# Kernel optimization log

Measured on AMD Instinct MI355X. Metric: run time of the kernel, lower is better.

## Reference

```python
import jax, jax.numpy as jnp
import numpy as np

N = 100_000      # nodes
E = 1_600_000    # edges (avg degree 16)
EP = 500_000     # pos/neg decode edges each
IN, H, OUT = 256, 128, 64


def setup_inputs() -> dict:
    key = jax.random.key(0)
    ks = jax.random.split(key, 8)
    x = jax.random.normal(ks[0], (N, IN), dtype=jnp.float32)
    edge_index = jax.random.randint(ks[1], (2, E), 0, N, dtype=jnp.int32)
    pos_edge_index = jax.random.randint(ks[2], (2, EP), 0, N, dtype=jnp.int32)
    neg_edge_index = jax.random.randint(ks[3], (2, EP), 0, N, dtype=jnp.int32)
    W1 = jax.random.normal(ks[4], (IN, H), dtype=jnp.float32) * (1.0 / np.sqrt(IN))
    b1 = jnp.zeros((H,), dtype=jnp.float32)
    W2 = jax.random.normal(ks[5], (H, OUT), dtype=jnp.float32) * (1.0 / np.sqrt(H))
    b2 = jnp.zeros((OUT,), dtype=jnp.float32)
    return dict(x=x, edge_index=edge_index, pos_edge_index=pos_edge_index,
                neg_edge_index=neg_edge_index, W1=W1, b1=b1, W2=W2, b2=b2)


def _gcn_conv(x, src, dst, norm, W, b, n_nodes):
    # PyG GCNConv: linear transform, then normalized scatter-add aggregation
    h = x @ W                              # [N, out]
    msg = h[src] * norm[:, None]           # gather + scale, [E+N, out]
    agg = jax.ops.segment_sum(msg, dst, num_segments=n_nodes)
    return agg + b


def reference(x, edge_index, pos_edge_index, neg_edge_index, W1, b1, W2, b2):
    n = x.shape[0]
    loops = jnp.arange(n, dtype=edge_index.dtype)
    src = jnp.concatenate([edge_index[0], loops])   # add self-loops (GCNConv default)
    dst = jnp.concatenate([edge_index[1], loops])
    # symmetric normalization D^{-1/2} (A+I) D^{-1/2}
    deg = jax.ops.segment_sum(jnp.ones_like(src, dtype=x.dtype), dst, num_segments=n)
    dinv = jnp.where(deg > 0, jax.lax.rsqrt(jnp.maximum(deg, 1e-12)), 0.0)
    norm = dinv[src] * dinv[dst]
    # encode
    h = jax.nn.relu(_gcn_conv(x, src, dst, norm, W1, b1, n))
    z = _gcn_conv(h, src, dst, norm, W2, b2, n)
    # decode: edge score = <z_u, z_v> over pos+neg edges
    ei = jnp.concatenate([pos_edge_index, neg_edge_index], axis=-1)
    return (z[ei[0]] * z[ei[1]]).sum(axis=-1)   # [2*EP]
```

## Files before the change

kernel.cpp:

```cpp
#include <hip/hip_runtime.h>


#define BUK_SHIFT 7
#define BUK_NODES 128

__global__ __launch_bounds__(256) void b_hist_k(const int* __restrict__ dst, int E,
                                                int nbuk, int* __restrict__ bhist) {
  __shared__ int h[1024];
  for (int i = threadIdx.x; i < nbuk; i += 256) h[i] = 0;
  __syncthreads();
  for (int i = blockIdx.x * 256 + threadIdx.x; i < E; i += gridDim.x * 256)
    atomicAdd(&h[dst[i] >> BUK_SHIFT], 1);
  __syncthreads();
  for (int i = threadIdx.x; i < nbuk; i += 256) {
    int c = h[i];
    if (c) atomicAdd(&bhist[i], c);
  }
}

__global__ __launch_bounds__(256) void b_scan_k(const int* __restrict__ bhist,
                                                int nbuk, int* __restrict__ bbase,
                                                int* __restrict__ bcur) {
  __shared__ int arr[256];
  const int t = threadIdx.x;
  const int per = (nbuk + 255) / 256;
  const int start = t * per;
  const int end = min(start + per, nbuk);
  int s = 0;
  for (int i = start; i < end; ++i) s += bhist[i];
  arr[t] = s;
  __syncthreads();
  for (int off = 1; off < 256; off <<= 1) {
    int v = (t >= off) ? arr[t - off] : 0;
    __syncthreads();
    arr[t] += v;
    __syncthreads();
  }
  int run = arr[t] - s;
  for (int i = start; i < end; ++i) {
    bbase[i] = run;
    bcur[i] = run;
    run += bhist[i];
  }
  if (t == 255) bbase[nbuk] = arr[255];
}

__global__ __launch_bounds__(256) void b_scatter_k(const int* __restrict__ src,
                                                   const int* __restrict__ dst, int E,
                                                   int nbuk, int* __restrict__ bcur,
                                                   int* __restrict__ ebuf) {
  __shared__ int lh[1024];
  __shared__ int lc[1024];
  const int base = blockIdx.x * 8192;
  if (base >= E) return;
  const int end = min(base + 8192, E);
  for (int i = threadIdx.x; i < nbuk; i += 256) lh[i] = 0;
  __syncthreads();
  for (int i = base + threadIdx.x; i < end; i += 256)
    atomicAdd(&lh[dst[i] >> BUK_SHIFT], 1);
  __syncthreads();
  for (int i = threadIdx.x; i < nbuk; i += 256) {
    int c = lh[i];
    lc[i] = c ? atomicAdd(&bcur[i], c) : 0;
  }
  __syncthreads();
  for (int i = base + threadIdx.x; i < end; i += 256) {
    int d = dst[i];
    int pos = atomicAdd(&lc[d >> BUK_SHIFT], 1);
    ebuf[pos] = src[i] | ((d & (BUK_NODES - 1)) << 17);
  }
}

__global__ __launch_bounds__(128) void b_build_k(const int* __restrict__ ebuf,
                                                 const int* __restrict__ bbase, int n,
                                                 int nbuk, float* __restrict__ dinv,
                                                 int* __restrict__ rowptr,
                                                 int* __restrict__ csr) {
  __shared__ int cnt[BUK_NODES];
  __shared__ int pre[BUK_NODES];
  __shared__ int cur[BUK_NODES];
  const int b = blockIdx.x, t = threadIdx.x;
  cnt[t] = 0;
  __syncthreads();
  const int beg = bbase[b], end = bbase[b + 1];
  for (int i = beg + t; i < end; i += 128) atomicAdd(&cnt[ebuf[i] >> 17], 1);
  __syncthreads();
  const int c = cnt[t];
  pre[t] = c;
  __syncthreads();
  for (int off = 1; off < 128; off <<= 1) {
    int v = (t >= off) ? pre[t - off] : 0;
    __syncthreads();
    pre[t] += v;
    __syncthreads();
  }
  const int base = beg + pre[t] - c;
  cur[t] = base;
  const int node = (b << BUK_SHIFT) + t;
  if (node < n) {
    rowptr[node] = base;
    dinv[node] = rsqrtf((float)(c + 1));
  }
  if (b == 0 && t == 0) rowptr[n] = bbase[nbuk];
  __syncthreads();
  for (int i = beg + t; i < end; i += 128) {
    int e = ebuf[i];
    int pos = atomicAdd(&cur[e >> 17], 1);
    csr[pos] = e & 0x1FFFF;
  }
}

template <int BM, int BN, int BK, int TM, int TN>
__global__ __launch_bounds__(256) void gemm_tiled(const float* __restrict__ A,
                                                  const float* __restrict__ B,
                                                  float* __restrict__ C,
                                                  const float* __restrict__ rowscale,
                                                  int M, int K) {
  __shared__ float As[BK][BM + 4];
  __shared__ float Bs[BK * BN];
  const int tid = threadIdx.x;
  const int tx = tid % (BN / TN);
  const int ty = tid / (BN / TN);
  const int lane = tid & 63;
  const int wave = tid >> 6;
  const int rowBase = blockIdx.x * BM;

  float acc[TM][TN];
#pragma unroll
  for (int i = 0; i < TM; ++i)
#pragma unroll
    for (int j = 0; j < TN; ++j) acc[i][j] = 0.f;

  constexpr int BS_BYTES = BK * BN * 4;
  constexpr int CALLS = BS_BYTES / 4096;

  for (int k0 = 0; k0 < K; k0 += BK) {
    {
      const char* gsrc = (const char*)(B + (size_t)k0 * BN);
#pragma unroll
      for (int q = 0; q < CALLS; ++q) {
        const int off = wave * (CALLS * 1024) + q * 1024 + lane * 16;
        __builtin_amdgcn_global_load_lds(
            (const __attribute__((address_space(1))) void*)(gsrc + off),
            (__attribute__((address_space(3))) void*)((char*)Bs + off), 16, 0, 0);
      }
    }
#pragma unroll
    for (int l = 0; l < BM * BK / (4 * 256); ++l) {
      const int idx = tid + l * 256;
      const int arow = idx / (BK / 4);
      const int acol = (idx % (BK / 4)) * 4;
      const int gr = rowBase + arow;
      float4 v;
      if (gr < M)
        v = *reinterpret_cast<const float4*>(&A[(size_t)gr * K + k0 + acol]);
      else
        v = make_float4(0.f, 0.f, 0.f, 0.f);
      As[acol + 0][arow] = v.x;
      As[acol + 1][arow] = v.y;
      As[acol + 2][arow] = v.z;
      As[acol + 3][arow] = v.w;
    }
    __syncthreads();
#pragma unroll
    for (int kk = 0; kk < BK; ++kk) {
      float ra[TM], rb[TN];
#pragma unroll
      for (int i = 0; i < TM; i += 4)
        *reinterpret_cast<float4*>(&ra[i]) =
            *reinterpret_cast<const float4*>(&As[kk][ty * TM + i]);
#pragma unroll
      for (int j = 0; j < TN; j += 4)
        *reinterpret_cast<float4*>(&rb[j]) =
            *reinterpret_cast<const float4*>(&Bs[kk * BN + tx * TN + j]);
#pragma unroll
      for (int i = 0; i < TM; ++i)
#pragma unroll
        for (int j = 0; j < TN; ++j) acc[i][j] += ra[i] * rb[j];
    }
    __syncthreads();
  }
#pragma unroll
  for (int i = 0; i < TM; ++i) {
    const int gr = rowBase + ty * TM + i;
    if (gr < M) {
      const float s = rowscale[gr];
#pragma unroll
      for (int j = 0; j < TN; j += 4) {
        float4 v = {acc[i][j] * s, acc[i][j + 1] * s, acc[i][j + 2] * s,
                    acc[i][j + 3] * s};
        *reinterpret_cast<float4*>(&C[(size_t)gr * BN + tx * TN + j]) = v;
      }
    }
  }
}

template <bool RELU>
__global__ __launch_bounds__(256) void agg128_k(const float* __restrict__ g,
                                                const int* __restrict__ rowptr,
                                                const int* __restrict__ csr,
                                                const float* __restrict__ dinv,
                                                const float* __restrict__ bias,
                                                float* __restrict__ hout, int n) {
  const int wid = (blockIdx.x * 256 + threadIdx.x) >> 6;
  if (wid >= n) return;
  const int lane = threadIdx.x & 63;
  const int half = lane >> 5;
  const size_t col = (size_t)(lane & 31) * 4;
  const float dd = dinv[wid];
  const int beg = rowptr[wid];
  const int end = rowptr[wid + 1];
  float4 acc = make_float4(0.f, 0.f, 0.f, 0.f);
  int e = beg;
  for (; e + 8 <= end; e += 8) {
    const int s0 = csr[e + 0 + half];
    const int s1 = csr[e + 2 + half];
    const int s2 = csr[e + 4 + half];
    const int s3 = csr[e + 6 + half];
    const float4 v0 = *reinterpret_cast<const float4*>(&g[(size_t)s0 * 128 + col]);
    const float4 v1 = *reinterpret_cast<const float4*>(&g[(size_t)s1 * 128 + col]);
    const float4 v2 = *reinterpret_cast<const float4*>(&g[(size_t)s2 * 128 + col]);
    const float4 v3 = *reinterpret_cast<const float4*>(&g[(size_t)s3 * 128 + col]);
    acc.x += (v0.x + v1.x) + (v2.x + v3.x);
    acc.y += (v0.y + v1.y) + (v2.y + v3.y);
    acc.z += (v0.z + v1.z) + (v2.z + v3.z);
    acc.w += (v0.w + v1.w) + (v2.w + v3.w);
  }
  for (; e + 2 <= end; e += 2) {
    const int s = csr[e + half];
    const float4 v = *reinterpret_cast<const float4*>(&g[(size_t)s * 128 + col]);
    acc.x += v.x;
    acc.y += v.y;
    acc.z += v.z;
    acc.w += v.w;
  }
  if (e < end && half == 0) {
    const int s = csr[e];
    const float4 v = *reinterpret_cast<const float4*>(&g[(size_t)s * 128 + col]);
    acc.x += v.x;
    acc.y += v.y;
    acc.z += v.z;
    acc.w += v.w;
  }
  acc.x += __shfl_xor(acc.x, 32);
  acc.y += __shfl_xor(acc.y, 32);
  acc.z += __shfl_xor(acc.z, 32);
  acc.w += __shfl_xor(acc.w, 32);
  if (half == 0) {
    const float4 sv = *reinterpret_cast<const float4*>(&g[(size_t)wid * 128 + col]);
    const float4 b = *reinterpret_cast<const float4*>(&bias[col]);
    float4 r;
    r.x = dd * (acc.x + sv.x) + b.x;
    r.y = dd * (acc.y + sv.y) + b.y;
    r.z = dd * (acc.z + sv.z) + b.z;
    r.w = dd * (acc.w + sv.w) + b.w;
    if (RELU) {
      r.x = fmaxf(r.x, 0.f);
      r.y = fmaxf(r.y, 0.f);
      r.z = fmaxf(r.z, 0.f);
      r.w = fmaxf(r.w, 0.f);
    }
    *reinterpret_cast<float4*>(&hout[(size_t)wid * 128 + col]) = r;
  }
}

__global__ __launch_bounds__(256) void agg64_k(const float* __restrict__ g,
                                               const int* __restrict__ rowptr,
                                               const int* __restrict__ csr,
                                               const float* __restrict__ dinv,
                                               const float* __restrict__ bias,
                                               float* __restrict__ hout, int n) {
  const int wid = (blockIdx.x * 256 + threadIdx.x) >> 6;
  if (wid >= n) return;
  const int lane = threadIdx.x & 63;
  const int quad = lane >> 4;
  const size_t col = (size_t)(lane & 15) * 4;
  const float dd = dinv[wid];
  const int beg = rowptr[wid];
  const int end = rowptr[wid + 1];
  float4 acc = make_float4(0.f, 0.f, 0.f, 0.f);
  int e = beg;
  for (; e + 16 <= end; e += 16) {
    const int s0 = csr[e + 0 + quad];
    const int s1 = csr[e + 4 + quad];
    const int s2 = csr[e + 8 + quad];
    const int s3 = csr[e + 12 + quad];
    const float4 v0 = *reinterpret_cast<const float4*>(&g[(size_t)s0 * 64 + col]);
    const float4 v1 = *reinterpret_cast<const float4*>(&g[(size_t)s1 * 64 + col]);
    const float4 v2 = *reinterpret_cast<const float4*>(&g[(size_t)s2 * 64 + col]);
    const float4 v3 = *reinterpret_cast<const float4*>(&g[(size_t)s3 * 64 + col]);
    acc.x += (v0.x + v1.x) + (v2.x + v3.x);
    acc.y += (v0.y + v1.y) + (v2.y + v3.y);
    acc.z += (v0.z + v1.z) + (v2.z + v3.z);
    acc.w += (v0.w + v1.w) + (v2.w + v3.w);
  }
  for (; e + 4 <= end; e += 4) {
    const int s = csr[e + quad];
    const float4 v = *reinterpret_cast<const float4*>(&g[(size_t)s * 64 + col]);
    acc.x += v.x;
    acc.y += v.y;
    acc.z += v.z;
    acc.w += v.w;
  }
  const int r = end - e;
  if (quad < r) {
    const int s = csr[e + quad];
    const float4 v = *reinterpret_cast<const float4*>(&g[(size_t)s * 64 + col]);
    acc.x += v.x;
    acc.y += v.y;
    acc.z += v.z;
    acc.w += v.w;
  }
  acc.x += __shfl_xor(acc.x, 16);
  acc.y += __shfl_xor(acc.y, 16);
  acc.z += __shfl_xor(acc.z, 16);
  acc.w += __shfl_xor(acc.w, 16);
  acc.x += __shfl_xor(acc.x, 32);
  acc.y += __shfl_xor(acc.y, 32);
  acc.z += __shfl_xor(acc.z, 32);
  acc.w += __shfl_xor(acc.w, 32);
  if (quad == 0) {
    const float4 sv = *reinterpret_cast<const float4*>(&g[(size_t)wid * 64 + col]);
    const float4 b = *reinterpret_cast<const float4*>(&bias[col]);
    float4 res;
    res.x = dd * (acc.x + sv.x) + b.x;
    res.y = dd * (acc.y + sv.y) + b.y;
    res.z = dd * (acc.z + sv.z) + b.z;
    res.w = dd * (acc.w + sv.w) + b.w;
    *reinterpret_cast<float4*>(&hout[(size_t)wid * 64 + col]) = res;
  }
}

__global__ __launch_bounds__(256) void decode_k(const int* __restrict__ pos,
                                                const int* __restrict__ neg,
                                                const float* __restrict__ z,
                                                float* __restrict__ out, int EP) {
  const long long t = (long long)blockIdx.x * 256 + threadIdx.x;
  const long long e = t >> 3;
  const int lane = (int)(t & 7);
  if (e >= 2LL * EP) return;
  int u, v;
  if (e < EP) {
    u = pos[e];
    v = pos[EP + e];
  } else {
    u = neg[e - EP];
    v = neg[EP + (e - EP)];
  }
  const float* zu = &z[(size_t)u * 64 + lane * 8];
  const float* zv = &z[(size_t)v * 64 + lane * 8];
  const float4 a0 = *reinterpret_cast<const float4*>(zu);
  const float4 a1 = *reinterpret_cast<const float4*>(zu + 4);
  const float4 b0 = *reinterpret_cast<const float4*>(zv);
  const float4 b1 = *reinterpret_cast<const float4*>(zv + 4);
  float p = a0.x * b0.x + a0.y * b0.y + a0.z * b0.z + a0.w * b0.w +
            a1.x * b1.x + a1.y * b1.y + a1.z * b1.z + a1.w * b1.w;
#pragma unroll
  for (int off = 4; off > 0; off >>= 1) p += __shfl_down(p, off, 8);
  if (lane == 0) out[e] = p;
}


extern "C" void kernel_launch(void* const* d_in, const int* in_sizes, int n_in,
                              void* d_out, int out_size, void* d_ws, size_t ws_size,
                              hipStream_t stream) {
  const float* x = (const float*)d_in[0];
  const int* ei = (const int*)d_in[1];
  const int* pos = (const int*)d_in[2];
  const int* neg = (const int*)d_in[3];
  const float* W1 = (const float*)d_in[4];
  const float* b1 = (const float*)d_in[5];
  const float* W2 = (const float*)d_in[6];
  const float* b2 = (const float*)d_in[7];
  float* out = (float*)d_out;

  const int H = in_sizes[5];
  const int IN = in_sizes[4] / H;
  const int OUT = in_sizes[7];
  const int N = in_sizes[0] / IN;
  const int E = in_sizes[1] / 2;
  const int EP = in_sizes[2] / 2;
  (void)OUT;

  char* ws = (char*)d_ws;
  size_t off = 0;
  auto carve = [&](size_t bytes) -> char* {
    char* p = ws + off;
    off += (bytes + 255) & ~(size_t)255;
    return p;
  };
  const int NBUK = (N + BUK_NODES - 1) >> BUK_SHIFT;

  float* dinvb = (float*)carve((size_t)N * 4);
  int* rowptr = (int*)carve((size_t)(N + 1) * 4);
  int* bhist = (int*)carve((size_t)NBUK * 4);
  int* bbase = (int*)carve((size_t)(NBUK + 1) * 4);
  int* bcur = (int*)carve((size_t)NBUK * 4);
  int* ebuf = (int*)carve((size_t)E * 4);
  int* csr = (int*)carve((size_t)E * 4);
  float* bufA = (float*)carve((size_t)N * H * 4);
  float* bufB = (float*)carve((size_t)N * H * 4);
  (void)ws_size;

  const int* srcp = ei;
  const int* dstp = ei + E;

  hipMemsetAsync(bhist, 0, (size_t)NBUK * 4, stream);
  b_hist_k<<<512, 256, 0, stream>>>(dstp, E, NBUK, bhist);
  b_scan_k<<<1, 256, 0, stream>>>(bhist, NBUK, bbase, bcur);
  b_scatter_k<<<(E + 8191) / 8192, 256, 0, stream>>>(srcp, dstp, E, NBUK, bcur, ebuf);
  b_build_k<<<NBUK, 128, 0, stream>>>(ebuf, bbase, N, NBUK, dinvb, rowptr, csr);

  gemm_tiled<64, 128, 32, 8, 4>
      <<<(N + 63) / 64, 256, 0, stream>>>(x, W1, bufA, dinvb, N, IN);
  agg128_k<true><<<(N + 3) / 4, 256, 0, stream>>>(bufA, rowptr, csr, dinvb, b1,
                                                  bufB, N);
  gemm_tiled<64, 64, 32, 4, 4>
      <<<(N + 63) / 64, 256, 0, stream>>>(bufB, W2, bufA, dinvb, N, H);
  agg64_k<<<(N + 3) / 4, 256, 0, stream>>>(bufA, rowptr, csr, dinvb, b2, bufB, N);
  const long long threads = 2LL * EP * 8;
  decode_k<<<(int)((threads + 255) / 256), 256, 0, stream>>>(pos, neg, bufB, out, EP);
}
```

Measured before the change: 430.6 us.

## Replace FP32 SIMT GEMMs with split-bf16 MFMA GEMMs

Both dense transforms now run on bf16 MFMA instructions, with an fp32-like result recovered by splitting each operand into hi and lo bf16 parts and issuing three MFMAs (hi*hi, lo*hi, hi*lo). The weights are pre-split and transposed by a small kernel launched on every call. A tiles are converted to hi/lo in registers before being stored to LDS. This targets the FP32 FMA throughput limit of the tiled SIMT GEMM, at the cost of extra conversion work, two extra tiny launches, and slightly different rounding.

```diff
diff --git a/kernel.cpp b/kernel.cpp
--- a/kernel.cpp
+++ b/kernel.cpp
@@ -1,5 +1,8 @@
 #include <hip/hip_runtime.h>
 
+
+typedef __attribute__((ext_vector_type(8))) short short8;
+typedef __attribute__((ext_vector_type(4))) float f32x4;
 
 #define BUK_SHIFT 7
 #define BUK_NODES 128
@@ -110,87 +113,107 @@
   }
 }
 
-template <int BM, int BN, int BK, int TM, int TN>
-__global__ __launch_bounds__(256) void gemm_tiled(const float* __restrict__ A,
-                                                  const float* __restrict__ B,
-                                                  float* __restrict__ C,
-                                                  const float* __restrict__ rowscale,
-                                                  int M, int K) {
-  __shared__ float As[BK][BM + 4];
-  __shared__ float Bs[BK * BN];
+__global__ __launch_bounds__(256) void split_w_k(const float* __restrict__ W, int K,
+                                                 int N,
+                                                 unsigned short* __restrict__ hi,
+                                                 unsigned short* __restrict__ lo) {
+  const int idx = blockIdx.x * 256 + threadIdx.x;
+  if (idx >= K * N) return;
+  const int k = idx / N, c = idx - k * N;
+  const float a = W[idx];
+  const unsigned u = __float_as_uint(a);
+  const unsigned short h = (unsigned short)(u >> 16);
+  const float l = a - __uint_as_float(u & 0xFFFF0000u);
+  const unsigned short lb = (unsigned short)(__float_as_uint(l) >> 16);
+  hi[(size_t)c * K + k] = h;
+  lo[(size_t)c * K + k] = lb;
+}
+
+template <int BN>
+__global__ __launch_bounds__(256) void gemm_mfma(
+    const float* __restrict__ A, const unsigned short* __restrict__ Bthi,
+    const unsigned short* __restrict__ Btlo, float* __restrict__ C,
+    const float* __restrict__ rowscale, int M, int K) {
+  constexpr int BM = 64, BK = 32;
+  constexpr int NT = BN / 16;
+  constexpr int LD = 40;
+  __shared__ unsigned short Ahi[BM * LD];
+  __shared__ unsigned short Alo[BM * LD];
+  __shared__ unsigned short Bhi[BN * LD];
+  __shared__ unsigned short Blo[BN * LD];
   const int tid = threadIdx.x;
-  const int tx = tid % (BN / TN);
-  const int ty = tid / (BN / TN);
   const int lane = tid & 63;
   const int wave = tid >> 6;
   const int rowBase = blockIdx.x * BM;
 
-  float acc[TM][TN];
-#pragma unroll
-  for (int i = 0; i < TM; ++i)
-#pragma unroll
-    for (int j = 0; j < TN; ++j) acc[i][j] = 0.f;
-
-  constexpr int BS_BYTES = BK * BN * 4;
-  constexpr int CALLS = BS_BYTES / 4096;
+  f32x4 acc[NT];
+#pragma unroll
+  for (int c = 0; c < NT; ++c) acc[c] = (f32x4){0.f, 0.f, 0.f, 0.f};
+
+  const int sr = tid >> 2;
+  const int sk = (tid & 3) * 8;
+  const int arow = wave * 16 + (lane & 15);
+  const int akb = (lane >> 4) * 8;
 
   for (int k0 = 0; k0 < K; k0 += BK) {
     {
-      const char* gsrc = (const char*)(B + (size_t)k0 * BN);
-#pragma unroll
-      for (int q = 0; q < CALLS; ++q) {
-        const int off = wave * (CALLS * 1024) + q * 1024 + lane * 16;
-        __builtin_amdgcn_global_load_lds(
-            (const __attribute__((address_space(1))) void*)(gsrc + off),
-            (__attribute__((address_space(3))) void*)((char*)Bs + off), 16, 0, 0);
+      const int gr = rowBase + sr;
+      float4 v0 = make_float4(0.f, 0.f, 0.f, 0.f);
+      float4 v1 = make_float4(0.f, 0.f, 0.f, 0.f);
+      if (gr < M) {
+        const float* p = A + (size_t)gr * K + k0 + sk;
+        v0 = *reinterpret_cast<const float4*>(p);
+        v1 = *reinterpret_cast<const float4*>(p + 4);
       }
+      const float vv[8] = {v0.x, v0.y, v0.z, v0.w, v1.x, v1.y, v1.z, v1.w};
+      short8 hv, lv;
+#pragma unroll
+      for (int i = 0; i < 8; ++i) {
+        const unsigned u = __float_as_uint(vv[i]);
+        hv[i] = (short)(u >> 16);
+        const float l = vv[i] - __uint_as_float(u & 0xFFFF0000u);
+        lv[i] = (short)(__float_as_uint(l) >> 16);
+      }
+      *reinterpret_cast<short8*>(&Ahi[sr * LD + sk]) = hv;
+      *reinterpret_cast<short8*>(&Alo[sr * LD + sk]) = lv;
     }
-#pragma unroll
-    for (int l = 0; l < BM * BK / (4 * 256); ++l) {
-      const int idx = tid + l * 256;
-      const int arow = idx / (BK / 4);
-      const int acol = (idx % (BK / 4)) * 4;
-      const int gr = rowBase + arow;
-      float4 v;
-      if (gr < M)
-        v = *reinterpret_cast<const float4*>(&A[(size_t)gr * K + k0 + acol]);
-      else
-        v = make_float4(0.f, 0.f, 0.f, 0.f);
-      As[acol + 0][arow] = v.x;
-      As[acol + 1][arow] = v.y;
-      As[acol + 2][arow] = v.z;
-      As[acol + 3][arow] = v.w;
+    for (int i = tid; i < BN * 2; i += 256) {
+      const int col = i >> 1;
+      const int kk = (i & 1) * 16;
+      const size_t gofs = (size_t)col * K + k0 + kk;
+      *reinterpret_cast<short8*>(&Bhi[col * LD + kk]) =
+          *reinterpret_cast<const short8*>(&Bthi[gofs]);
+      *reinterpret_cast<short8*>(&Bhi[col * LD + kk + 8]) =
+          *reinterpret_cast<const short8*>(&Bthi[gofs + 8]);
+      *reinterpret_cast<short8*>(&Blo[col * LD + kk]) =
+          *reinterpret_cast<const short8*>(&Btlo[gofs]);
+      *reinterpret_cast<short8*>(&Blo[col * LD + kk + 8]) =
+          *reinterpret_cast<const short8*>(&Btlo[gofs + 8]);
     }
     __syncthreads();
-#pragma unroll
-    for (int kk = 0; kk < BK; ++kk) {
-      float ra[TM], rb[TN];
-#pragma unroll
-      for (int i = 0; i < TM; i += 4)
-        *reinterpret_cast<float4*>(&ra[i]) =
-            *reinterpret_cast<const float4*>(&As[kk][ty * TM + i]);
-#pragma unroll
-      for (int j = 0; j < TN; j += 4)
-        *reinterpret_cast<float4*>(&rb[j]) =
-            *reinterpret_cast<const float4*>(&Bs[kk * BN + tx * TN + j]);
-#pragma unroll
-      for (int i = 0; i < TM; ++i)
-#pragma unroll
-        for (int j = 0; j < TN; ++j) acc[i][j] += ra[i] * rb[j];
+    const short8 fa_hi = *reinterpret_cast<const short8*>(&Ahi[arow * LD + akb]);
+    const short8 fa_lo = *reinterpret_cast<const short8*>(&Alo[arow * LD + akb]);
+#pragma unroll
+    for (int c = 0; c < NT; ++c) {
+      const int bofs = (c * 16 + (lane & 15)) * LD + akb;
+      const short8 fb_hi = *reinterpret_cast<const short8*>(&Bhi[bofs]);
+      const short8 fb_lo = *reinterpret_cast<const short8*>(&Blo[bofs]);
+      acc[c] = __builtin_amdgcn_mfma_f32_16x16x32_bf16(fa_hi, fb_hi, acc[c], 0, 0, 0);
+      acc[c] = __builtin_amdgcn_mfma_f32_16x16x32_bf16(fa_lo, fb_hi, acc[c], 0, 0, 0);
+      acc[c] = __builtin_amdgcn_mfma_f32_16x16x32_bf16(fa_hi, fb_lo, acc[c], 0, 0, 0);
     }
     __syncthreads();
   }
-#pragma unroll
-  for (int i = 0; i < TM; ++i) {
-    const int gr = rowBase + ty * TM + i;
-    if (gr < M) {
-      const float s = rowscale[gr];
-#pragma unroll
-      for (int j = 0; j < TN; j += 4) {
-        float4 v = {acc[i][j] * s, acc[i][j + 1] * s, acc[i][j + 2] * s,
-                    acc[i][j + 3] * s};
-        *reinterpret_cast<float4*>(&C[(size_t)gr * BN + tx * TN + j]) = v;
-      }
+  const int crow = rowBase + wave * 16 + (lane >> 4) * 4;
+  float sc[4];
+#pragma unroll
+  for (int j = 0; j < 4; ++j) sc[j] = (crow + j < M) ? rowscale[crow + j] : 0.f;
+#pragma unroll
+  for (int c = 0; c < NT; ++c) {
+#pragma unroll
+    for (int j = 0; j < 4; ++j) {
+      const int gr = crow + j;
+      if (gr < M) C[(size_t)gr * BN + c * 16 + (lane & 15)] = acc[c][j] * sc[j];
     }
   }
 }
@@ -380,7 +403,6 @@
   const int N = in_sizes[0] / IN;
   const int E = in_sizes[1] / 2;
   const int EP = in_sizes[2] / 2;
-  (void)OUT;
 
   char* ws = (char*)d_ws;
   size_t off = 0;
@@ -400,10 +422,17 @@
   int* csr = (int*)carve((size_t)E * 4);
   float* bufA = (float*)carve((size_t)N * H * 4);
   float* bufB = (float*)carve((size_t)N * H * 4);
+  unsigned short* w1hi = (unsigned short*)carve((size_t)IN * H * 2);
+  unsigned short* w1lo = (unsigned short*)carve((size_t)IN * H * 2);
+  unsigned short* w2hi = (unsigned short*)carve((size_t)H * OUT * 2);
+  unsigned short* w2lo = (unsigned short*)carve((size_t)H * OUT * 2);
   (void)ws_size;
 
   const int* srcp = ei;
   const int* dstp = ei + E;
+
+  split_w_k<<<(IN * H + 255) / 256, 256, 0, stream>>>(W1, IN, H, w1hi, w1lo);
+  split_w_k<<<(H * OUT + 255) / 256, 256, 0, stream>>>(W2, H, OUT, w2hi, w2lo);
 
   hipMemsetAsync(bhist, 0, (size_t)NBUK * 4, stream);
   b_hist_k<<<512, 256, 0, stream>>>(dstp, E, NBUK, bhist);
@@ -411,12 +440,10 @@
   b_scatter_k<<<(E + 8191) / 8192, 256, 0, stream>>>(srcp, dstp, E, NBUK, bcur, ebuf);
   b_build_k<<<NBUK, 128, 0, stream>>>(ebuf, bbase, N, NBUK, dinvb, rowptr, csr);
 
-  gemm_tiled<64, 128, 32, 8, 4>
-      <<<(N + 63) / 64, 256, 0, stream>>>(x, W1, bufA, dinvb, N, IN);
+  gemm_mfma<128><<<(N + 63) / 64, 256, 0, stream>>>(x, w1hi, w1lo, bufA, dinvb, N, IN);
   agg128_k<true><<<(N + 3) / 4, 256, 0, stream>>>(bufA, rowptr, csr, dinvb, b1,
                                                   bufB, N);
-  gemm_tiled<64, 64, 32, 4, 4>
-      <<<(N + 63) / 64, 256, 0, stream>>>(bufB, W2, bufA, dinvb, N, H);
+  gemm_mfma<64><<<(N + 63) / 64, 256, 0, stream>>>(bufB, w2hi, w2lo, bufA, dinvb, N, H);
   agg64_k<<<(N + 3) / 4, 256, 0, stream>>>(bufA, rowptr, csr, dinvb, b2, bufB, N);
   const long long threads = 2LL * EP * 8;
   decode_k<<<(int)((threads + 255) / 256), 256, 0, stream>>>(pos, neg, bufB, out, EP);
```

Measured after the change: 377.7 us. -12.3%, faster.
